# Kernel optimization log

Hardware: AMD Instinct MI355X
Metric: run time of the kernel (lower is better)

## Reference

```python
import jax, jax.numpy as jnp
import numpy as np

THRESH = 1e-6
EPS = 1e-8
LN_EPS = 1e-5


def _layer(h, M, W_in, b_in, W_out, b_out, W_self, b_self, gamma, beta):
    # Normalize incoming flows per destination column: A[j,i] = M[j,i]/sum_k M[k,i]
    A = M / (jnp.sum(M, axis=0, keepdims=True) + EPS)
    mask = A > THRESH
    W = jnp.where(mask, A, 0.0)                      # thresholded edge weights [N,N]
    T = h @ W_in + b_in                              # transformed features [N,out]
    weighted_sum = jnp.einsum('ji,jd->id', W, T)     # sum over origins j per dest i
    weight_sum = jnp.sum(W, axis=0)                  # [N]
    has_edge = jnp.any(mask, axis=0)                 # dest i has >=1 incoming edge
    agg = jnp.where(has_edge[:, None],
                    weighted_sum / (weight_sum[:, None] + EPS),
                    T)
    agg = agg @ W_out + b_out                        # dropout is identity in eval
    out = agg + (h @ W_self + b_self)                # residual (dims differ -> self_transform)
    mu = jnp.mean(out, axis=-1, keepdims=True)
    var = jnp.mean(jnp.square(out - mu), axis=-1, keepdims=True)
    out = (out - mu) * jax.lax.rsqrt(var + LN_EPS) * gamma + beta
    return out


def setup_inputs() -> dict:
    key = jax.random.key(0)
    ks = jax.random.split(key, 16)
    N, D_IN, D_H, D_OUT = 8192, 256, 512, 256
    s = 0.05
    return {
        'node_features': jax.random.normal(ks[0], (N, D_IN), jnp.float32),
        'mobility_matrix': jax.random.uniform(ks[1], (N, N), jnp.float32),
        # layer 1: in -> hidden
        'W_in1': jax.random.normal(ks[2], (D_IN, D_H)) * s,
        'b_in1': jnp.zeros((D_H,)),
        'W_out1': jax.random.normal(ks[3], (D_H, D_H)) * s,
        'b_out1': jnp.zeros((D_H,)),
        'W_self1': jax.random.normal(ks[4], (D_IN, D_H)) * s,
        'b_self1': jnp.zeros((D_H,)),
        'g1': jnp.ones((D_H,)),
        'be1': jnp.zeros((D_H,)),
        # layer 2: hidden -> out
        'W_in2': jax.random.normal(ks[5], (D_H, D_OUT)) * s,
        'b_in2': jnp.zeros((D_OUT,)),
        'W_out2': jax.random.normal(ks[6], (D_OUT, D_OUT)) * s,
        'b_out2': jnp.zeros((D_OUT,)),
        'W_self2': jax.random.normal(ks[7], (D_H, D_OUT)) * s,
        'b_self2': jnp.zeros((D_OUT,)),
        'g2': jnp.ones((D_OUT,)),
        'be2': jnp.zeros((D_OUT,)),
    }


def reference(node_features, mobility_matrix,
              W_in1, b_in1, W_out1, b_out1, W_self1, b_self1, g1, be1,
              W_in2, b_in2, W_out2, b_out2, W_self2, b_self2, g2, be2):
    h = _layer(node_features, mobility_matrix,
               W_in1, b_in1, W_out1, b_out1, W_self1, b_self1, g1, be1)
    h = jax.nn.relu(h)  # inter-layer activation
    h = _layer(h, mobility_matrix,
               W_in2, b_in2, W_out2, b_out2, W_self2, b_self2, g2, be2)
    h = jax.nn.relu(h)  # final activation
    return h
```

## Files before the change

kernel.cpp:

```cpp
#include <hip/hip_runtime.h>
#include <stdint.h>

typedef short bf16x8 __attribute__((ext_vector_type(8)));
typedef short s16x4 __attribute__((ext_vector_type(4)));
typedef float f32x4 __attribute__((ext_vector_type(4)));
typedef unsigned int u32;

#define EPS_A 1e-8f
#define THR_A 1e-6f
#define NN 8192

static __device__ __forceinline__ short f2bf(float f) {
  u32 u = __float_as_uint(f);
  u = u + 0x7FFFu + ((u >> 16) & 1u);
  return (short)(u >> 16);
}
static __device__ __forceinline__ float bf2f(short s) {
  return __uint_as_float(((u32)(unsigned short)s) << 16);
}
static __device__ __forceinline__ void gld16(const short* g, short* l) {
  __builtin_amdgcn_global_load_lds(
      (const __attribute__((address_space(1))) u32*)g,
      (__attribute__((address_space(3))) u32*)l, 16, 0, 0);
}

__global__ __launch_bounds__(256) void k_prep_all(
    const float* __restrict__ Mob, const float* __restrict__ nf,
    const float* __restrict__ W_in1, const float* __restrict__ W_out1,
    const float* __restrict__ W_self1, const float* __restrict__ W_in2,
    const float* __restrict__ W_out2, const float* __restrict__ W_self2,
    const float* __restrict__ b_in1, const float* __restrict__ b_out1,
    const float* __restrict__ b_self1, const float* __restrict__ b_out2,
    const float* __restrict__ b_self2,
    short* __restrict__ Mt, float* __restrict__ colsum, u32* __restrict__ colmax,
    short* __restrict__ nft, short* __restrict__ A1cat, short* __restrict__ Win1b,
    short* __restrict__ Wout1t, short* __restrict__ Bcat1, short* __restrict__ Win2t,
    short* __restrict__ Bcat2, float* __restrict__ bias1c, float* __restrict__ bias2c)
{
  __shared__ __align__(16) short sbuf[256 * 66];
  int b = blockIdx.x;
  const int t = threadIdx.x;
  if (b < 4096) {
    const int i0 = (b & 31) * 256;
    const int j0 = (b >> 5) * 64;
    const int i = i0 + t;
    float s = 0.f, mx = 0.f;
    #pragma unroll 4
    for (int jj = 0; jj < 64; ++jj) {
      float v = Mob[(size_t)(j0 + jj) * NN + i];
      s += v;
      mx = fmaxf(mx, v);
      sbuf[t * 66 + jj] = f2bf(v);
    }
    atomicAdd(&colsum[i], s);
    atomicMax(&colmax[i], __float_as_uint(mx));
    __syncthreads();
    #pragma unroll
    for (int p = 0; p < 8; ++p) {
      const int r = p * 32 + (t >> 3);
      const int c = t & 7;
      const u32* src = (const u32*)((const char*)sbuf + r * 132 + c * 16);
      int4 w = make_int4(src[0], src[1], src[2], src[3]);
      *(int4*)((char*)Mt + (((size_t)(i0 + r) * NN + j0) * 2 + c * 16)) = w;
    }
    return;
  }
  b -= 4096;
  if (b < 512) {
    short (*tile)[65] = (short(*)[65])sbuf;
    const int r0 = (b & 127) * 64, c0 = (b >> 7) * 64;
    #pragma unroll
    for (int p = 0; p < 16; ++p) {
      const int rr = p * 4 + (t >> 6), cc = t & 63;
      tile[rr][cc] = f2bf(nf[(size_t)(r0 + rr) * 256 + c0 + cc]);
    }
    __syncthreads();
    #pragma unroll
    for (int q = 0; q < 16; ++q) {
      const int cc = q * 4 + (t >> 6), rr = t & 63;
      nft[(size_t)(c0 + cc) * 8192 + r0 + rr] = tile[rr][cc];
    }
    return;
  }
  b -= 512;
  if (b < 2048) {
    const int idx = b * 256 + t;
    const float4 v = ((const float4*)nf)[idx];
    const int i = idx >> 6;
    const int c = (idx & 63) * 4;
    s16x4 o;
    o.x = f2bf(v.x); o.y = f2bf(v.y); o.z = f2bf(v.z); o.w = f2bf(v.w);
    *(s16x4*)&A1cat[(size_t)i * 512 + 256 + c] = o;
    return;
  }
  b -= 2048;
  if (b < 128) {
    const int idx = b * 256 + t;
    const float4 v = ((const float4*)W_in1)[idx];
    s16x4 o;
    o.x = f2bf(v.x); o.y = f2bf(v.y); o.z = f2bf(v.z); o.w = f2bf(v.w);
    *(s16x4*)&Win1b[idx * 4] = o;
    return;
  }
  b -= 128;
  if (b < 1024) {
    const int idx = b * 256 + t;
    const int r = idx >> 9, c = idx & 511;
    Wout1t[(size_t)c * 512 + r] = f2bf(W_out1[idx]);
    return;
  }
  b -= 1024;
  if (b < 512) {
    const int idx = b * 256 + t;
    const int r = idx >> 9, c = idx & 511;
    Bcat1[(size_t)c * 512 + 256 + r] = f2bf(W_self1[idx]);
    return;
  }
  b -= 512;
  if (b < 512) {
    const int idx = b * 256 + t;
    const int r = idx >> 8, c = idx & 255;
    Win2t[(size_t)c * 512 + r] = f2bf(W_in2[idx]);
    return;
  }
  b -= 512;
  if (b < 256) {
    const int idx = b * 256 + t;
    const int r = idx >> 8, c = idx & 255;
    Bcat2[(size_t)c * 768 + r] = f2bf(W_out2[idx]);
    return;
  }
  b -= 256;
  if (b < 512) {
    const int idx = b * 256 + t;
    const int r = idx >> 8, c = idx & 255;
    Bcat2[(size_t)c * 768 + 256 + r] = f2bf(W_self2[idx]);
    return;
  }
  b -= 512;
  if (b < 2) {
    const int n = b * 256 + t;
    float a = b_out1[n] + b_self1[n];
    for (int p = 0; p < 512; ++p) a += b_in1[p] * W_out1[(size_t)p * 512 + n];
    bias1c[n] = a;
    return;
  }
  bias2c[t] = b_out2[t] + b_self2[t];
}

__global__ __launch_bounds__(256) void k_gemm_raw_n(
    const short* __restrict__ A, const short* __restrict__ B, int K, int ldA, int ldB,
    short* __restrict__ C, int ldC)
{
  constexpr int LDP = 40;
  __shared__ __align__(16) short As[64 * LDP];
  __shared__ __align__(16) short Bs[64 * LDP];
  const int t = threadIdx.x;
  const int m0 = blockIdx.y * 64, n0 = blockIdx.x * 64;
  const int wid = t >> 6, l = t & 63;
  const int wr = wid >> 1, wc = wid & 1;
  const int lr = l & 15, lk = l >> 4;
  f32x4 acc[2][2] = {};
  const int sr = t >> 2;
  const int sc = (t & 3) * 8;
  const short* gA0 = A + (size_t)(m0 + sr) * ldA + sc;
  const short* gB0 = B + (size_t)(n0 + sr) * ldB + sc;
  for (int k0 = 0; k0 < K; k0 += 32) {
    const int4 a0 = *(const int4*)(gA0 + k0);
    const int4 b0 = *(const int4*)(gB0 + k0);
    __syncthreads();
    *(int4*)&As[sr * LDP + sc] = a0;
    *(int4*)&Bs[sr * LDP + sc] = b0;
    __syncthreads();
    bf16x8 av[2], bv[2];
    #pragma unroll
    for (int mi = 0; mi < 2; ++mi)
      av[mi] = *(const bf16x8*)&As[(wr * 32 + mi * 16 + lr) * LDP + lk * 8];
    #pragma unroll
    for (int ni = 0; ni < 2; ++ni)
      bv[ni] = *(const bf16x8*)&Bs[(wc * 32 + ni * 16 + lr) * LDP + lk * 8];
    #pragma unroll
    for (int mi = 0; mi < 2; ++mi)
      #pragma unroll
      for (int ni = 0; ni < 2; ++ni)
        acc[mi][ni] = __builtin_amdgcn_mfma_f32_16x16x32_bf16(av[mi], bv[ni], acc[mi][ni], 0, 0, 0);
  }
  #pragma unroll
  for (int mi = 0; mi < 2; ++mi)
    #pragma unroll
    for (int r = 0; r < 4; ++r) {
      const int m = m0 + wr * 32 + mi * 16 + lk * 4 + r;
      #pragma unroll
      for (int ni = 0; ni < 2; ++ni) {
        const int n = n0 + wc * 32 + ni * 16 + lr;
        C[(size_t)m * ldC + n] = f2bf(acc[mi][ni][r]);
      }
    }
}

template <int BN, int EPI>
__global__ __launch_bounds__(256) void k_g64(
    const short* __restrict__ A, const short* __restrict__ B, int K, int ldA, int ldB,
    void* __restrict__ Cout, int ldC, const float* __restrict__ bias0)
{
  constexpr int ROWS = 64 + BN;
  constexpr int CH = ROWS / 32;
  constexpr int NI = BN / 32;
  __shared__ __align__(16) short S[ROWS * 64];
  const int t = threadIdx.x;

  const int gx = gridDim.x;
  int flat = blockIdx.y * gx + blockIdx.x;
  const int cpx = (gx * gridDim.y) >> 3;
  flat = (flat & 7) * cpx + (flat >> 3);
  const int bx = flat % gx, by = flat / gx;
  const int m0 = by * 64, n0 = bx * BN;

  const int wid = t >> 6, l = t & 63;
  const int wr = wid >> 1, wc = wid & 1;
  const int lr = l & 15, lk = l >> 4;

  f32x4 acc[2][NI] = {};

  const int lrow = l >> 3, lcol = l & 7;
  const int wbase = wid * (ROWS / 4);
  short* dbase = S + wbase * 64;
  const short* gsrc[CH];
  #pragma unroll
  for (int c = 0; c < CH; ++c) {
    const int ar = wbase + c * 8 + lrow;
    const int scol = (lcol ^ (ar & 7)) * 8;
    gsrc[c] = (ar < 64) ? A + (size_t)(m0 + ar) * ldA + scol
                        : B + (size_t)(n0 + ar - 64) * ldB + scol;
  }

  const int niters = K >> 6;
  int kk = flat % niters;
  for (int it = 0; it < niters; ++it) {
    const int koff = kk << 6;
    kk = (kk + 1 == niters) ? 0 : kk + 1;
    __syncthreads();
    #pragma unroll
    for (int c = 0; c < CH; ++c)
      gld16(gsrc[c] + koff, dbase + c * 512);
    __syncthreads();

    __builtin_amdgcn_s_setprio(1);
    #pragma unroll
    for (int ks = 0; ks < 2; ++ks) {
      bf16x8 av[2], bv[NI];
      #pragma unroll
      for (int mi = 0; mi < 2; ++mi) {
        const int row = wr * 32 + mi * 16 + lr;
        av[mi] = *(const bf16x8*)&S[row * 64 + ((ks * 4 + lk) ^ (row & 7)) * 8];
      }
      #pragma unroll
      for (int ni = 0; ni < NI; ++ni) {
        const int row = 64 + wc * (BN / 2) + ni * 16 + lr;
        bv[ni] = *(const bf16x8*)&S[row * 64 + ((ks * 4 + lk) ^ (row & 7)) * 8];
      }
      #pragma unroll
      for (int mi = 0; mi < 2; ++mi)
        #pragma unroll
        for (int ni = 0; ni < NI; ++ni)
          acc[mi][ni] = __builtin_amdgcn_mfma_f32_16x16x32_bf16(av[mi], bv[ni], acc[mi][ni], 0, 0, 0);
    }
    __builtin_amdgcn_s_setprio(0);
  }

  #pragma unroll
  for (int mi = 0; mi < 2; ++mi) {
    #pragma unroll
    for (int r = 0; r < 4; ++r) {
      const int m = m0 + wr * 32 + mi * 16 + lk * 4 + r;
      float bm = 0.f;
      if (EPI == 0) bm = bias0[m];
      #pragma unroll
      for (int ni = 0; ni < NI; ++ni) {
        const int n = n0 + wc * (BN / 2) + ni * 16 + lr;
        float v = acc[mi][ni][r];
        if (EPI == 0) ((short*)Cout)[(size_t)m * ldC + n] = f2bf(v + bm);
        else          ((float*)Cout)[(size_t)m * ldC + n] = v + bias0[n];
      }
    }
  }
}

__global__ __launch_bounds__(256) void k_gemm_sk128(
    const short* __restrict__ A, const short* __restrict__ B, int K, int ldA, int ldB,
    short* __restrict__ P, int ldC, size_t pstride)
{
  __shared__ __align__(16) short As[128 * 64];
  __shared__ __align__(16) short Bs[128 * 64];
  const int t = threadIdx.x;

  const int sk = blockIdx.z;
  A += (size_t)sk * K;
  B += (size_t)sk * K;

  const int gx = gridDim.x;
  int flat = blockIdx.y * gx + blockIdx.x;
  const int cpx = (gx * gridDim.y) >> 3;
  flat = (flat & 7) * cpx + (flat >> 3);
  const int bx = flat % gx, by = flat / gx;
  const int m0 = by * 128, n0 = bx * 128;

  const int wid = t >> 6, l = t & 63;
  const int wr = wid >> 1, wc = wid & 1;
  const int lr = l & 15, lk = l >> 4;

  f32x4 acc[4][4] = {};

  const int side = wid >> 1;
  const int hrow = (wid & 1) * 64;
  const short* Xp = side ? B : A;
  const int ldX = side ? ldB : ldA;
  const int x0 = side ? n0 : m0;
  short* dbase = (side ? Bs : As) + hrow * 64;
  const int lrow = l >> 3, lcol = l & 7;
  const short* g0 = Xp + (size_t)(x0 + hrow + lrow) * ldX + (lcol ^ lrow) * 8;
  const size_t st8 = (size_t)8 * ldX;

  const int niters = K >> 6;
  int kk = (flat + sk * 3) & (niters - 1);

  for (int it = 0; it < niters; ++it) {
    const int koff = kk << 6;
    kk = (kk + 1) & (niters - 1);
    __syncthreads();
    gld16(g0 + koff,            dbase);
    gld16(g0 + koff + st8,      dbase + 512);
    gld16(g0 + koff + 2 * st8,  dbase + 1024);
    gld16(g0 + koff + 3 * st8,  dbase + 1536);
    gld16(g0 + koff + 4 * st8,  dbase + 2048);
    gld16(g0 + koff + 5 * st8,  dbase + 2560);
    gld16(g0 + koff + 6 * st8,  dbase + 3072);
    gld16(g0 + koff + 7 * st8,  dbase + 3584);
    __syncthreads();

    __builtin_amdgcn_s_setprio(1);
    #pragma unroll
    for (int ks = 0; ks < 2; ++ks) {
      bf16x8 av[4], bv[4];
      #pragma unroll
      for (int mi = 0; mi < 4; ++mi) {
        const int row = wr * 64 + mi * 16 + lr;
        av[mi] = *(const bf16x8*)&As[row * 64 + ((ks * 4 + lk) ^ (lr & 7)) * 8];
      }
      #pragma unroll
      for (int ni = 0; ni < 4; ++ni) {
        const int row = wc * 64 + ni * 16 + lr;
        bv[ni] = *(const bf16x8*)&Bs[row * 64 + ((ks * 4 + lk) ^ (lr & 7)) * 8];
      }
      #pragma unroll
      for (int mi = 0; mi < 4; ++mi)
        #pragma unroll
        for (int ni = 0; ni < 4; ++ni)
          acc[mi][ni] = __builtin_amdgcn_mfma_f32_16x16x32_bf16(av[mi], bv[ni], acc[mi][ni], 0, 0, 0);
    }
    __builtin_amdgcn_s_setprio(0);
  }

  short* outp = P + pstride * sk;
  #pragma unroll
  for (int mi = 0; mi < 4; ++mi) {
    #pragma unroll
    for (int r = 0; r < 4; ++r) {
      const int m = m0 + wr * 64 + mi * 16 + lk * 4 + r;
      #pragma unroll
      for (int ni = 0; ni < 4; ++ni) {
        const int n = n0 + wc * 64 + ni * 16 + lr;
        outp[(size_t)m * ldC + n] = f2bf(acc[mi][ni][r]);
      }
    }
  }
}

__global__ __launch_bounds__(256) void k_sk_reduce_sub(
    const short* __restrict__ P, int N, size_t pstride, int S,
    const float* __restrict__ colsum, const u32* __restrict__ colmax,
    const short* __restrict__ hraw, int ldh,
    short* __restrict__ out, int ldo)
{
  const int idx = blockIdx.x * 256 + threadIdx.x;
  const int nq = N >> 2;
  const int m = idx / nq;
  const int c4 = (idx - m * nq) * 4;
  const size_t base = (size_t)m * N + c4;
  float a0 = 0.f, a1 = 0.f, a2 = 0.f, a3 = 0.f;
  for (int s = 0; s < S; ++s) {
    s16x4 v = *(const s16x4*)&P[pstride * s + base];
    a0 += bf2f(v.x); a1 += bf2f(v.y); a2 += bf2f(v.z); a3 += bf2f(v.w);
  }
  const float cs = colsum[m];
  const float rc = 1.f / (cs + EPS_A);
  const float rcw = rc / (cs * rc + EPS_A);
  const bool he = __uint_as_float(colmax[m]) * rc > THR_A;
  s16x4 o;
  if (he) {
    o.x = f2bf(a0 * rcw); o.y = f2bf(a1 * rcw);
    o.z = f2bf(a2 * rcw); o.w = f2bf(a3 * rcw);
  } else {
    o = *(const s16x4*)&hraw[(size_t)m * ldh + c4];
  }
  *(s16x4*)&out[(size_t)m * ldo + c4] = o;
}

__global__ __launch_bounds__(256) void k_sk_reduce(
    const short* __restrict__ P, int N, size_t pstride, int S,
    const float* __restrict__ colsum, const u32* __restrict__ colmax,
    const short* __restrict__ Tfall, short* __restrict__ out, int ldo)
{
  const int idx = blockIdx.x * 256 + threadIdx.x;
  const int nq = N >> 2;
  const int m = idx / nq;
  const int c4 = (idx - m * nq) * 4;
  const size_t base = (size_t)m * N + c4;
  float a0 = 0.f, a1 = 0.f, a2 = 0.f, a3 = 0.f;
  for (int s = 0; s < S; ++s) {
    s16x4 v = *(const s16x4*)&P[pstride * s + base];
    a0 += bf2f(v.x); a1 += bf2f(v.y); a2 += bf2f(v.z); a3 += bf2f(v.w);
  }
  const float cs = colsum[m];
  const float rc = 1.f / (cs + EPS_A);
  const float rcw = rc / (cs * rc + EPS_A);
  const bool he = __uint_as_float(colmax[m]) * rc > THR_A;
  a0 *= rcw; a1 *= rcw; a2 *= rcw; a3 *= rcw;
  if (__ballot(!he)) {
    if (!he) {
      a0 = bf2f(Tfall[(size_t)(c4 + 0) * NN + m]);
      a1 = bf2f(Tfall[(size_t)(c4 + 1) * NN + m]);
      a2 = bf2f(Tfall[(size_t)(c4 + 2) * NN + m]);
      a3 = bf2f(Tfall[(size_t)(c4 + 3) * NN + m]);
    }
  }
  s16x4 o;
  o.x = f2bf(a0); o.y = f2bf(a1); o.z = f2bf(a2); o.w = f2bf(a3);
  *(s16x4*)&out[(size_t)m * ldo + c4] = o;
}

template <int MODE>
__device__ __forceinline__ void ln_relu_body(
    const float* __restrict__ X, int W,
    const float* __restrict__ g, const float* __restrict__ be,
    void* __restrict__ out, int ldo)
{
  const int row = blockIdx.x;
  const int t = threadIdx.x;
  const float* x = X + (size_t)row * W;
  float v0 = x[t], v1 = 0.f;
  float s = v0, ss = v0 * v0;
  if (W == 512) { v1 = x[t + 256]; s += v1; ss += v1 * v1; }
  #pragma unroll
  for (int off = 32; off; off >>= 1) {
    s += __shfl_down(s, off);
    ss += __shfl_down(ss, off);
  }
  __shared__ float red[8];
  const int wid = t >> 6;
  if ((t & 63) == 0) { red[wid] = s; red[4 + wid] = ss; }
  __syncthreads();
  s = red[0] + red[1] + red[2] + red[3];
  ss = red[4] + red[5] + red[6] + red[7];
  const float mu = s / W;
  const float var = ss / W - mu * mu;
  const float sc = rsqrtf(var + 1e-5f);
  float y = fmaxf((v0 - mu) * sc * g[t] + be[t], 0.f);
  if (MODE == 0) ((short*)out)[(size_t)row * ldo + t] = f2bf(y);
  else           ((float*)out)[(size_t)row * ldo + t] = y;
  if (W == 512) {
    float y1 = fmaxf((v1 - mu) * sc * g[t + 256] + be[t + 256], 0.f);
    if (MODE == 0) ((short*)out)[(size_t)row * ldo + t + 256] = f2bf(y1);
    else           ((float*)out)[(size_t)row * ldo + t + 256] = y1;
  }
}

__global__ __launch_bounds__(256) void k_ln_relu_bf16(
    const float* __restrict__ X, int W, const float* __restrict__ g,
    const float* __restrict__ be, short* __restrict__ out, int ldo) {
  ln_relu_body<0>(X, W, g, be, out, ldo);
}
__global__ __launch_bounds__(256) void k_ln_relu_f32(
    const float* __restrict__ X, int W, const float* __restrict__ g,
    const float* __restrict__ be, float* __restrict__ out, int ldo) {
  ln_relu_body<1>(X, W, g, be, out, ldo);
}

extern "C" void kernel_launch(void* const* d_in, const int* in_sizes, int n_in,
                              void* d_out, int out_size, void* d_ws, size_t ws_size,
                              hipStream_t stream) {
  const float* nf      = (const float*)d_in[0];
  const float* Mob     = (const float*)d_in[1];
  const float* W_in1   = (const float*)d_in[2];
  const float* b_in1   = (const float*)d_in[3];
  const float* W_out1  = (const float*)d_in[4];
  const float* b_out1  = (const float*)d_in[5];
  const float* W_self1 = (const float*)d_in[6];
  const float* b_self1 = (const float*)d_in[7];
  const float* g1      = (const float*)d_in[8];
  const float* be1     = (const float*)d_in[9];
  const float* W_in2   = (const float*)d_in[10];
  const float* b_in2   = (const float*)d_in[11];
  const float* W_out2  = (const float*)d_in[12];
  const float* b_out2  = (const float*)d_in[13];
  const float* W_self2 = (const float*)d_in[14];
  const float* b_self2 = (const float*)d_in[15];
  const float* g2      = (const float*)d_in[16];
  const float* be2     = (const float*)d_in[17];

  char* ws = (char*)d_ws;
  float* colsum = (float*)(ws);
  u32*   colmax = (u32*)(ws + 32768);
  short* Mt     = (short*)(ws + 131072);
  short* nft    = (short*)(ws + 134348800);
  short* A1cat  = (short*)(ws + 138543104);
  float* C2f    = (float*)(ws + 146931712);
  short* Acat2  = (short*)(ws + 163708928);
  short* T2t    = (short*)(ws + 176291840);
  short* Bcat1  = (short*)(ws + 180486144);
  short* Bcat2  = (short*)(ws + 181010432);
  short* Win2t  = (short*)(ws + 181403648);
  short* Wout1t = (short*)(ws + 181665792);
  short* Win1b  = (short*)(ws + 182190080);
  float* bias1c = (float*)(ws + 182452224);
  float* bias2c = (float*)(ws + 182454272);
  short* P1     = (short*)(ws + 188743680);
  short* P2     = (short*)(ws + 222298112);

  hipMemsetAsync(ws, 0, 65536, stream);

  k_prep_all<<<9603, 256, 0, stream>>>(Mob, nf, W_in1, W_out1, W_self1, W_in2,
                                       W_out2, W_self2, b_in1, b_out1, b_self1,
                                       b_out2, b_self2, Mt, colsum, colmax, nft,
                                       A1cat, Win1b, Wout1t, Bcat1, Win2t, Bcat2,
                                       bias1c, bias2c);
  k_gemm_raw_n<<<dim3(4, 8), 256, 0, stream>>>(Wout1t, Win1b, 512, 512, 512,
                                               Bcat1, 512);

  k_gemm_sk128<<<dim3(2, 64, 8), 256, 0, stream>>>(Mt, nft, 1024, NN, NN,
                                                   P1, 256, (size_t)8192 * 256);
  k_sk_reduce_sub<<<2048, 256, 0, stream>>>(P1, 256, (size_t)8192 * 256, 8,
                                            colsum, colmax, A1cat + 256, 512,
                                            A1cat, 512);
  k_g64<128, 2><<<dim3(4, 128), 256, 0, stream>>>(A1cat, Bcat1, 512, 512, 512,
                                                  C2f, 512, bias1c);
  k_ln_relu_bf16<<<8192, 256, 0, stream>>>(C2f, 512, g1, be1, Acat2 + 256, 768);

  k_g64<64, 0><<<dim3(128, 4), 256, 0, stream>>>(Win2t, Acat2 + 256, 512, 512, 768,
                                                 T2t, NN, b_in2);
  k_gemm_sk128<<<dim3(2, 64, 8), 256, 0, stream>>>(Mt, T2t, 1024, NN, NN,
                                                   P2, 256, (size_t)8192 * 256);
  k_sk_reduce<<<2048, 256, 0, stream>>>(P2, 256, (size_t)8192 * 256, 8,
                                        colsum, colmax, T2t, Acat2, 768);
  k_g64<64, 2><<<dim3(4, 128), 256, 0, stream>>>(Acat2, Bcat2, 768, 768, 768,
                                                 C2f, 256, bias2c);
  k_ln_relu_f32<<<8192, 256, 0, stream>>>(C2f, 256, g2, be2, (float*)d_out, 256);
}
```

Before: 298.3 us.

## Switch big aggregation GEMMs to FP8 operands for mobility matrix and features

Stores the transposed mobility matrix, transposed node features and layer-2 transformed features as FP8 instead of BF16, and runs the two split-K aggregation GEMMs with fp8 MFMA. The LDS tiling and swizzle are reworked for byte-sized elements, and the T2 GEMM epilogue gains a variant that also emits an FP8 copy. The aim is to halve the memory traffic of the 8192x8192 matrix, both when it is written in prep and when it is read twice, and to use the faster FP8 MFMA rate. In exchange, precision drops noticeably, since FP8 e4m3 has about a 3-bit mantissa, so tolerance failures are a risk.

```diff
diff --git a/kernel.cpp b/kernel.cpp
--- a/kernel.cpp
+++ b/kernel.cpp
@@ -5,6 +5,7 @@
 typedef short s16x4 __attribute__((ext_vector_type(4)));
 typedef float f32x4 __attribute__((ext_vector_type(4)));
 typedef unsigned int u32;
+typedef unsigned char u8;
 
 #define EPS_A 1e-8f
 #define THR_A 1e-6f
@@ -18,7 +19,10 @@
 static __device__ __forceinline__ float bf2f(short s) {
   return __uint_as_float(((u32)(unsigned short)s) << 16);
 }
-static __device__ __forceinline__ void gld16(const short* g, short* l) {
+static __device__ __forceinline__ u8 f2fp8(float v) {
+  return (u8)(__builtin_amdgcn_cvt_pk_fp8_f32(v, v, 0, false) & 0xff);
+}
+static __device__ __forceinline__ void gld16(const void* g, void* l) {
   __builtin_amdgcn_global_load_lds(
       (const __attribute__((address_space(1))) u32*)g,
       (__attribute__((address_space(3))) u32*)l, 16, 0, 0);
@@ -32,12 +36,12 @@
     const float* __restrict__ b_in1, const float* __restrict__ b_out1,
     const float* __restrict__ b_self1, const float* __restrict__ b_out2,
     const float* __restrict__ b_self2,
-    short* __restrict__ Mt, float* __restrict__ colsum, u32* __restrict__ colmax,
-    short* __restrict__ nft, short* __restrict__ A1cat, short* __restrict__ Win1b,
+    u8* __restrict__ Mt8, float* __restrict__ colsum, u32* __restrict__ colmax,
+    u8* __restrict__ nft8, short* __restrict__ A1cat, short* __restrict__ Win1b,
     short* __restrict__ Wout1t, short* __restrict__ Bcat1, short* __restrict__ Win2t,
     short* __restrict__ Bcat2, float* __restrict__ bias1c, float* __restrict__ bias2c)
 {
-  __shared__ __align__(16) short sbuf[256 * 66];
+  __shared__ __align__(16) u32 sbuf[256 * 17];
   int b = blockIdx.x;
   const int t = threadIdx.x;
   if (b < 4096) {
@@ -46,39 +50,44 @@
     const int i = i0 + t;
     float s = 0.f, mx = 0.f;
     #pragma unroll 4
-    for (int jj = 0; jj < 64; ++jj) {
-      float v = Mob[(size_t)(j0 + jj) * NN + i];
-      s += v;
-      mx = fmaxf(mx, v);
-      sbuf[t * 66 + jj] = f2bf(v);
+    for (int j4 = 0; j4 < 16; ++j4) {
+      float v0 = Mob[(size_t)(j0 + j4 * 4 + 0) * NN + i];
+      float v1 = Mob[(size_t)(j0 + j4 * 4 + 1) * NN + i];
+      float v2 = Mob[(size_t)(j0 + j4 * 4 + 2) * NN + i];
+      float v3 = Mob[(size_t)(j0 + j4 * 4 + 3) * NN + i];
+      s += v0 + v1 + v2 + v3;
+      mx = fmaxf(fmaxf(mx, fmaxf(v0, v1)), fmaxf(v2, v3));
+      u32 pk = __builtin_amdgcn_cvt_pk_fp8_f32(v0, v1, 0, false);
+      pk = __builtin_amdgcn_cvt_pk_fp8_f32(v2, v3, (int)pk, true);
+      sbuf[t * 17 + j4] = pk;
     }
     atomicAdd(&colsum[i], s);
     atomicMax(&colmax[i], __float_as_uint(mx));
     __syncthreads();
     #pragma unroll
-    for (int p = 0; p < 8; ++p) {
-      const int r = p * 32 + (t >> 3);
-      const int c = t & 7;
-      const u32* src = (const u32*)((const char*)sbuf + r * 132 + c * 16);
+    for (int p = 0; p < 4; ++p) {
+      const int r = p * 64 + (t >> 2);
+      const int c = t & 3;
+      const u32* src = &sbuf[r * 17 + c * 4];
       int4 w = make_int4(src[0], src[1], src[2], src[3]);
-      *(int4*)((char*)Mt + (((size_t)(i0 + r) * NN + j0) * 2 + c * 16)) = w;
+      *(int4*)&Mt8[(size_t)(i0 + r) * NN + j0 + c * 16] = w;
     }
     return;
   }
   b -= 4096;
   if (b < 512) {
-    short (*tile)[65] = (short(*)[65])sbuf;
+    u8* tile = (u8*)sbuf;
     const int r0 = (b & 127) * 64, c0 = (b >> 7) * 64;
     #pragma unroll
     for (int p = 0; p < 16; ++p) {
       const int rr = p * 4 + (t >> 6), cc = t & 63;
-      tile[rr][cc] = f2bf(nf[(size_t)(r0 + rr) * 256 + c0 + cc]);
+      tile[rr * 68 + cc] = f2fp8(nf[(size_t)(r0 + rr) * 256 + c0 + cc]);
     }
     __syncthreads();
     #pragma unroll
     for (int q = 0; q < 16; ++q) {
       const int cc = q * 4 + (t >> 6), rr = t & 63;
-      nft[(size_t)(c0 + cc) * 8192 + r0 + rr] = tile[rr][cc];
+      nft8[(size_t)(c0 + cc) * 8192 + r0 + rr] = tile[rr * 68 + cc];
     }
     return;
   }
@@ -201,7 +210,8 @@
 template <int BN, int EPI>
 __global__ __launch_bounds__(256) void k_g64(
     const short* __restrict__ A, const short* __restrict__ B, int K, int ldA, int ldB,
-    void* __restrict__ Cout, int ldC, const float* __restrict__ bias0)
+    void* __restrict__ Cout, int ldC, const float* __restrict__ bias0,
+    u8* __restrict__ C8)
 {
   constexpr int ROWS = 64 + BN;
   constexpr int CH = ROWS / 32;
@@ -274,24 +284,29 @@
     for (int r = 0; r < 4; ++r) {
       const int m = m0 + wr * 32 + mi * 16 + lk * 4 + r;
       float bm = 0.f;
-      if (EPI == 0) bm = bias0[m];
+      if (EPI == 0 || EPI == 4) bm = bias0[m];
       #pragma unroll
       for (int ni = 0; ni < NI; ++ni) {
         const int n = n0 + wc * (BN / 2) + ni * 16 + lr;
         float v = acc[mi][ni][r];
-        if (EPI == 0) ((short*)Cout)[(size_t)m * ldC + n] = f2bf(v + bm);
-        else          ((float*)Cout)[(size_t)m * ldC + n] = v + bias0[n];
-      }
-    }
-  }
-}
-
-__global__ __launch_bounds__(256) void k_gemm_sk128(
-    const short* __restrict__ A, const short* __restrict__ B, int K, int ldA, int ldB,
+        if (EPI == 0 || EPI == 4) {
+          v += bm;
+          ((short*)Cout)[(size_t)m * ldC + n] = f2bf(v);
+          if (EPI == 4) C8[(size_t)m * ldC + n] = f2fp8(v);
+        } else {
+          ((float*)Cout)[(size_t)m * ldC + n] = v + bias0[n];
+        }
+      }
+    }
+  }
+}
+
+__global__ __launch_bounds__(256) void k_sk128_f8(
+    const u8* __restrict__ A, const u8* __restrict__ B, int K, int ldA, int ldB,
     short* __restrict__ P, int ldC, size_t pstride)
 {
-  __shared__ __align__(16) short As[128 * 64];
-  __shared__ __align__(16) short Bs[128 * 64];
+  __shared__ __align__(16) u8 As[128 * 64];
+  __shared__ __align__(16) u8 Bs[128 * 64];
   const int t = threadIdx.x;
 
   const int sk = blockIdx.z;
@@ -313,50 +328,51 @@
 
   const int side = wid >> 1;
   const int hrow = (wid & 1) * 64;
-  const short* Xp = side ? B : A;
+  const u8* Xp = side ? B : A;
   const int ldX = side ? ldB : ldA;
   const int x0 = side ? n0 : m0;
-  short* dbase = (side ? Bs : As) + hrow * 64;
-  const int lrow = l >> 3, lcol = l & 7;
-  const short* g0 = Xp + (size_t)(x0 + hrow + lrow) * ldX + (lcol ^ lrow) * 8;
-  const size_t st8 = (size_t)8 * ldX;
+  u8* dbase = (side ? Bs : As) + hrow * 64;
+  const u8* gsrc[4];
+  #pragma unroll
+  for (int c = 0; c < 4; ++c) {
+    const int row = hrow + c * 16 + (l >> 2);
+    const int ql = (l & 3) ^ (row & 3);
+    gsrc[c] = Xp + (size_t)(x0 + row) * ldX + ql * 16;
+  }
 
   const int niters = K >> 6;
   int kk = (flat + sk * 3) & (niters - 1);
-
   for (int it = 0; it < niters; ++it) {
     const int koff = kk << 6;
     kk = (kk + 1) & (niters - 1);
     __syncthreads();
-    gld16(g0 + koff,            dbase);
-    gld16(g0 + koff + st8,      dbase + 512);
-    gld16(g0 + koff + 2 * st8,  dbase + 1024);
-    gld16(g0 + koff + 3 * st8,  dbase + 1536);
-    gld16(g0 + koff + 4 * st8,  dbase + 2048);
-    gld16(g0 + koff + 5 * st8,  dbase + 2560);
-    gld16(g0 + koff + 6 * st8,  dbase + 3072);
-    gld16(g0 + koff + 7 * st8,  dbase + 3584);
+    gld16(gsrc[0] + koff, dbase);
+    gld16(gsrc[1] + koff, dbase + 1024);
+    gld16(gsrc[2] + koff, dbase + 2048);
+    gld16(gsrc[3] + koff, dbase + 3072);
     __syncthreads();
 
     __builtin_amdgcn_s_setprio(1);
     #pragma unroll
     for (int ks = 0; ks < 2; ++ks) {
-      bf16x8 av[4], bv[4];
+      const int q = ks * 2 + (lk >> 1);
+      const int inner = (lk & 1) * 8;
+      long av[4], bv[4];
       #pragma unroll
       for (int mi = 0; mi < 4; ++mi) {
         const int row = wr * 64 + mi * 16 + lr;
-        av[mi] = *(const bf16x8*)&As[row * 64 + ((ks * 4 + lk) ^ (lr & 7)) * 8];
+        av[mi] = *(const long*)&As[row * 64 + ((q ^ (row & 3)) << 4) + inner];
       }
       #pragma unroll
       for (int ni = 0; ni < 4; ++ni) {
         const int row = wc * 64 + ni * 16 + lr;
-        bv[ni] = *(const bf16x8*)&Bs[row * 64 + ((ks * 4 + lk) ^ (lr & 7)) * 8];
+        bv[ni] = *(const long*)&Bs[row * 64 + ((q ^ (row & 3)) << 4) + inner];
       }
       #pragma unroll
       for (int mi = 0; mi < 4; ++mi)
         #pragma unroll
         for (int ni = 0; ni < 4; ++ni)
-          acc[mi][ni] = __builtin_amdgcn_mfma_f32_16x16x32_bf16(av[mi], bv[ni], acc[mi][ni], 0, 0, 0);
+          acc[mi][ni] = __builtin_amdgcn_mfma_f32_16x16x32_fp8_fp8(av[mi], bv[ni], acc[mi][ni], 0, 0, 0);
     }
     __builtin_amdgcn_s_setprio(0);
   }
@@ -511,48 +527,49 @@
   char* ws = (char*)d_ws;
   float* colsum = (float*)(ws);
   u32*   colmax = (u32*)(ws + 32768);
-  short* Mt     = (short*)(ws + 131072);
-  short* nft    = (short*)(ws + 134348800);
-  short* A1cat  = (short*)(ws + 138543104);
-  float* C2f    = (float*)(ws + 146931712);
-  short* Acat2  = (short*)(ws + 163708928);
-  short* T2t    = (short*)(ws + 176291840);
-  short* Bcat1  = (short*)(ws + 180486144);
-  short* Bcat2  = (short*)(ws + 181010432);
-  short* Win2t  = (short*)(ws + 181403648);
-  short* Wout1t = (short*)(ws + 181665792);
-  short* Win1b  = (short*)(ws + 182190080);
-  float* bias1c = (float*)(ws + 182452224);
-  float* bias2c = (float*)(ws + 182454272);
-  short* P1     = (short*)(ws + 188743680);
-  short* P2     = (short*)(ws + 222298112);
+  u8*    Mt8    = (u8*)(ws + 131072);
+  u8*    nft8   = (u8*)(ws + 67239936);
+  u8*    T2t8   = (u8*)(ws + 69337088);
+  short* A1cat  = (short*)(ws + 71434240);
+  float* C2f    = (float*)(ws + 79822848);
+  short* Acat2  = (short*)(ws + 96600064);
+  short* T2t    = (short*)(ws + 109182976);
+  short* Bcat1  = (short*)(ws + 113377280);
+  short* Bcat2  = (short*)(ws + 113901568);
+  short* Win2t  = (short*)(ws + 114294784);
+  short* Wout1t = (short*)(ws + 114556928);
+  short* Win1b  = (short*)(ws + 115081216);
+  float* bias1c = (float*)(ws + 115343360);
+  float* bias2c = (float*)(ws + 115345408);
+  short* P1     = (short*)(ws + 117440512);
+  short* P2     = (short*)(ws + 150994944);
 
   hipMemsetAsync(ws, 0, 65536, stream);
 
   k_prep_all<<<9603, 256, 0, stream>>>(Mob, nf, W_in1, W_out1, W_self1, W_in2,
                                        W_out2, W_self2, b_in1, b_out1, b_self1,
-                                       b_out2, b_self2, Mt, colsum, colmax, nft,
+                                       b_out2, b_self2, Mt8, colsum, colmax, nft8,
                                        A1cat, Win1b, Wout1t, Bcat1, Win2t, Bcat2,
                                        bias1c, bias2c);
   k_gemm_raw_n<<<dim3(4, 8), 256, 0, stream>>>(Wout1t, Win1b, 512, 512, 512,
                                                Bcat1, 512);
 
-  k_gemm_sk128<<<dim3(2, 64, 8), 256, 0, stream>>>(Mt, nft, 1024, NN, NN,
-                                                   P1, 256, (size_t)8192 * 256);
+  k_sk128_f8<<<dim3(2, 64, 8), 256, 0, stream>>>(Mt8, nft8, 1024, NN, NN,
+                                                 P1, 256, (size_t)8192 * 256);
   k_sk_reduce_sub<<<2048, 256, 0, stream>>>(P1, 256, (size_t)8192 * 256, 8,
                                             colsum, colmax, A1cat + 256, 512,
                                             A1cat, 512);
   k_g64<128, 2><<<dim3(4, 128), 256, 0, stream>>>(A1cat, Bcat1, 512, 512, 512,
-                                                  C2f, 512, bias1c);
+                                                  C2f, 512, bias1c, nullptr);
   k_ln_relu_bf16<<<8192, 256, 0, stream>>>(C2f, 512, g1, be1, Acat2 + 256, 768);
 
-  k_g64<64, 0><<<dim3(128, 4), 256, 0, stream>>>(Win2t, Acat2 + 256, 512, 512, 768,
-                                                 T2t, NN, b_in2);
-  k_gemm_sk128<<<dim3(2, 64, 8), 256, 0, stream>>>(Mt, T2t, 1024, NN, NN,
-                                                   P2, 256, (size_t)8192 * 256);
+  k_g64<64, 4><<<dim3(128, 4), 256, 0, stream>>>(Win2t, Acat2 + 256, 512, 512, 768,
+                                                 T2t, NN, b_in2, T2t8);
+  k_sk128_f8<<<dim3(2, 64, 8), 256, 0, stream>>>(Mt8, T2t8, 1024, NN, NN,
+                                                 P2, 256, (size_t)8192 * 256);
   k_sk_reduce<<<2048, 256, 0, stream>>>(P2, 256, (size_t)8192 * 256, 8,
                                         colsum, colmax, T2t, Acat2, 768);
   k_g64<64, 2><<<dim3(4, 128), 256, 0, stream>>>(Acat2, Bcat2, 768, 768, 768,
-                                                 C2f, 256, bias2c);
+                                                 C2f, 256, bias2c, nullptr);
   k_ln_relu_f32<<<8192, 256, 0, stream>>>(C2f, 256, g2, be2, (float*)d_out, 256);
 }
```

Measured after the change: 278.9 us. -6.5%, faster.
